# Kernel optimization log

Hardware: AMD Instinct MI355X
Metric: run time of the kernel (lower is better)

The kernel has to match this reference:

```python
import jax, jax.numpy as jnp
import numpy as np

B = 32768
INPUT_DIM = 2048
D = 2
HIDDEN = 128
V = 20          # output_dim (number of heads)
P = 6           # n_corr_params
R = 10          # r_lora = min(V // 2, 10)


def setup_inputs() -> dict:
    key = jax.random.key(0)
    ks = jax.random.split(key, 12)

    def lin(k, fan_in, shape):
        bound = 1.0 / np.sqrt(fan_in)
        return jax.random.uniform(k, shape, jnp.float32, -bound, bound)

    x = jax.random.normal(ks[0], (B, INPUT_DIM), jnp.float32)
    # encoder: Linear(input_dim, hidden) -> ReLU -> (Dropout=id) -> Linear(hidden, d)
    We1 = lin(ks[1], INPUT_DIM, (INPUT_DIM, HIDDEN))
    be1 = lin(ks[2], INPUT_DIM, (HIDDEN,))
    We2 = lin(ks[3], HIDDEN, (HIDDEN, D))
    be2 = lin(ks[4], HIDDEN, (D,))
    # 20 heads, each Linear(d, hidden) -> ReLU -> Linear(hidden, 6) -> Tanh,
    # stacked into batched weight tensors.
    W1 = lin(ks[5], D, (V, D, HIDDEN))
    b1 = lin(ks[6], D, (V, HIDDEN))
    W2 = lin(ks[7], HIDDEN, (V, HIDDEN, P))
    b2 = lin(ks[8], HIDDEN, (V, P))
    # LoRA params
    lora_A = jax.random.normal(ks[9], (D, R), jnp.float32) * 0.01
    lora_B = jax.random.normal(ks[10], (R, V * P), jnp.float32) * 0.01
    return {"x": x, "We1": We1, "be1": be1, "We2": We2, "be2": be2,
            "W1": W1, "b1": b1, "W2": W2, "b2": b2,
            "lora_A": lora_A, "lora_B": lora_B}


def reference(x, We1, be1, We2, be2, W1, b1, W2, b2, lora_A, lora_B):
    # encoder (nonlinear reduction; dropout is identity in eval)
    z = jax.nn.relu(x @ We1 + be1) @ We2 + be2            # [B, D]
    # all 20 heads as batched GEMMs
    h = jax.nn.relu(jnp.einsum('bd,vdh->bvh', z, W1) + b1)  # [B, V, HIDDEN]
    heads = jnp.tanh(jnp.einsum('bvh,vhp->bvp', h, W2) + b2)  # [B, V, P]
    # LoRA contribution, then outer tanh (note: double tanh, faithful to source)
    lora = (z @ lora_A @ lora_B).reshape(-1, V, P)         # [B, V, P]
    out = jnp.tanh(heads + 0.15 * lora)
    return (out, z)
```

## Files before the change

### kernel.cpp

```cpp
#include <hip/hip_runtime.h>
#include <hip/hip_bf16.h>
#include <cstdint>
#include <cstddef>

#define BDIM   32768
#define KDIM   2048
#define NDIM   128
#define VHEADS 20
#define PDIM   6
#define RLORA  10

#define BK      64
#define NCHUNK  (KDIM / BK)
#define OUT_ELEMS   (BDIM * VHEADS * PDIM)
#define WS_W_BYTES  (KDIM * NDIM * 2)

typedef __attribute__((ext_vector_type(8))) __bf16 bf16x8;
typedef __attribute__((ext_vector_type(4))) float f32x4;
typedef __attribute__((ext_vector_type(2))) float f32x2;
typedef __attribute__((ext_vector_type(4))) unsigned int u32x4;

union FragU { bf16x8 b; u32x4 u; };

__device__ __forceinline__ unsigned int cvt_pk_bf16(float lo, float hi) {
  unsigned int r;
  asm("v_cvt_pk_bf16_f32 %0, %1, %2" : "=v"(r) : "v"(lo), "v"(hi));
  return r;
}

__device__ __forceinline__ void gload_lds16(const void* g, void* l) {
  __builtin_amdgcn_global_load_lds(
      (const __attribute__((address_space(1))) void*)(g),
      (__attribute__((address_space(3))) void*)(l), 16, 0, 0);
}

__device__ __forceinline__ float fast_tanh(float x) {
  float ax = fabsf(x);
  float e  = __expf(-2.0f * ax);
  float t  = __fdividef(1.0f - e, 1.0f + e);
  return copysignf(t, x);
}

__global__ __launch_bounds__(256)
void k0_pack(const float* __restrict__ We1,
             const float* __restrict__ lA,
             const float* __restrict__ lB,
             unsigned short* __restrict__ wsw,
             float* __restrict__ wsM) {
  if (blockIdx.x == 128) {
    int t = threadIdx.x;
    if (t < 2 * VHEADS * PDIM) {
      int d  = t / (VHEADS * PDIM);
      int vp = t - d * (VHEADS * PDIM);
      float s = 0.f;
#pragma unroll
      for (int r = 0; r < RLORA; ++r)
        s = fmaf(lA[d * RLORA + r], lB[r * (VHEADS * PDIM) + vp], s);
      wsM[t] = s;
    }
    return;
  }
  int t    = blockIdx.x * 256 + threadIdx.x;
  int lane = t & 63;
  int blk  = t >> 6;
  int ks   = blk & 1;
  int nt   = (blk >> 1) & 7;
  int c    = blk >> 4;
  int n    = nt * 16 + (lane & 15);
  int kb   = c * 64 + ks * 32 + (lane >> 4) * 8;

  unsigned int u[4];
#pragma unroll
  for (int q = 0; q < 4; ++q) {
    float f0 = We1[(size_t)(kb + 2 * q + 0) * NDIM + n];
    float f1 = We1[(size_t)(kb + 2 * q + 1) * NDIM + n];
    __hip_bfloat16 h0 = __float2bfloat16(f0);
    __hip_bfloat16 h1 = __float2bfloat16(f1);
    u[q] = (unsigned int)*reinterpret_cast<unsigned short*>(&h0) |
           ((unsigned int)*reinterpret_cast<unsigned short*>(&h1) << 16);
  }
  *reinterpret_cast<u32x4*>(wsw + (size_t)t * 8) = u32x4{u[0], u[1], u[2], u[3]};
}

__global__ __launch_bounds__(256, 2)
void k1_fused(const float* __restrict__ x,
              const unsigned short* __restrict__ wp,
              const float* __restrict__ be1,
              const float* __restrict__ We2,
              const float* __restrict__ be2,
              const float* __restrict__ W1,
              const float* __restrict__ b1,
              const float* __restrict__ W2,
              const float* __restrict__ b2,
              const float* __restrict__ M,
              float* __restrict__ out,
              float* __restrict__ zout) {
  __shared__ char ldsA[2][16384] __attribute__((aligned(16)));
  __shared__ char ldsB[2][16384] __attribute__((aligned(16)));
  __shared__ float zsh[64][2];

  const int tid  = threadIdx.x;
  const int lane = tid & 63;
  const int wv   = tid >> 6;
  const int l15  = lane & 15;
  const int kgrp = lane >> 4;
  const int blk  = blockIdx.x;

  const int arow_off = wv * 16 + (lane >> 4);
  const char* bsrc = (const char*)wp + lane * 16;

  f32x4 acc[8];
#pragma unroll
  for (int i = 0; i < 8; ++i) acc[i] = f32x4{0.f, 0.f, 0.f, 0.f};

  auto STAGE = [&](int b, int c) {
#pragma unroll
    for (int q = 0; q < 4; ++q) {
      int row = arow_off + q * 4;
      const float* asrc = x + ((size_t)(blk * 64 + row) * KDIM + c * BK
                               + (((l15 ^ (row & 7)) << 2)));
      gload_lds16(asrc, &ldsA[b][(wv * 4 + q) * 1024]);
    }
#pragma unroll
    for (int q = 0; q < 4; ++q) {
      gload_lds16(bsrc + (size_t)c * 16384 + (wv * 4 + q) * 1024,
                  &ldsB[b][(wv * 4 + q) * 1024]);
    }
  };

  auto COMPUTE = [&](int b) {
    const int row = wv * 16 + l15;
    const char* abase = &ldsA[b][row * 256];
    const int rx = (row & 7) << 4;
    f32x4 A0 = *(const f32x4*)(abase + (((kgrp * 2 + 0) << 4) ^ rx));
    f32x4 A1 = *(const f32x4*)(abase + (((kgrp * 2 + 1) << 4) ^ rx));
    f32x4 A2 = *(const f32x4*)(abase + 128 + (((kgrp * 2 + 0) << 4) ^ rx));
    f32x4 A3 = *(const f32x4*)(abase + 128 + (((kgrp * 2 + 1) << 4) ^ rx));
    FragU a0, a1;
    a0.u = u32x4{cvt_pk_bf16(A0.x, A0.y), cvt_pk_bf16(A0.z, A0.w),
                 cvt_pk_bf16(A1.x, A1.y), cvt_pk_bf16(A1.z, A1.w)};
    a1.u = u32x4{cvt_pk_bf16(A2.x, A2.y), cvt_pk_bf16(A2.z, A2.w),
                 cvt_pk_bf16(A3.x, A3.y), cvt_pk_bf16(A3.z, A3.w)};
    const char* bbase = &ldsB[b][lane * 16];
#pragma unroll
    for (int nt = 0; nt < 8; ++nt) {
      FragU b0, b1;
      b0.u = *(const u32x4*)(bbase + (nt * 2 + 0) * 1024);
      b1.u = *(const u32x4*)(bbase + (nt * 2 + 1) * 1024);
      acc[nt] = __builtin_amdgcn_mfma_f32_16x16x32_bf16(a0.b, b0.b, acc[nt], 0, 0, 0);
      acc[nt] = __builtin_amdgcn_mfma_f32_16x16x32_bf16(a1.b, b1.b, acc[nt], 0, 0, 0);
    }
  };

  STAGE(0, 0);
  STAGE(1, 1);

#pragma unroll 1
  for (int c = 0; c < NCHUNK; ++c) {
    int b = c & 1;
    if (c + 1 < NCHUNK) {
      asm volatile("s_waitcnt vmcnt(8)" ::: "memory");
    } else {
      asm volatile("s_waitcnt vmcnt(0)" ::: "memory");
    }
    __builtin_amdgcn_sched_barrier(0);
    __builtin_amdgcn_s_barrier();
    COMPUTE(b);
    __builtin_amdgcn_s_barrier();
    __builtin_amdgcn_sched_barrier(0);
    if (c + 2 < NCHUNK) STAGE(b, c + 2);
  }

  float part[4][2];
#pragma unroll
  for (int j = 0; j < 4; ++j) { part[j][0] = 0.f; part[j][1] = 0.f; }
#pragma unroll
  for (int nt = 0; nt < 8; ++nt) {
    int col = nt * 16 + l15;
    float bb = be1[col];
    float w0 = We2[col * 2 + 0];
    float w1 = We2[col * 2 + 1];
#pragma unroll
    for (int j = 0; j < 4; ++j) {
      float h = acc[nt][j] + bb;
      h = h > 0.f ? h : 0.f;
      part[j][0] = fmaf(h, w0, part[j][0]);
      part[j][1] = fmaf(h, w1, part[j][1]);
    }
  }
#pragma unroll
  for (int m = 1; m < 16; m <<= 1) {
#pragma unroll
    for (int j = 0; j < 4; ++j) {
      part[j][0] += __shfl_xor(part[j][0], m, 64);
      part[j][1] += __shfl_xor(part[j][1], m, 64);
    }
  }
  if (l15 == 0) {
    float bz0 = be2[0], bz1 = be2[1];
#pragma unroll
    for (int j = 0; j < 4; ++j) {
      int rl = wv * 16 + kgrp * 4 + j;
      float zz0 = part[j][0] + bz0;
      float zz1 = part[j][1] + bz1;
      zsh[rl][0] = zz0;
      zsh[rl][1] = zz1;
      f32x2 zz = {zz0, zz1};
      *(f32x2*)(zout + (size_t)(blk * 64 + rl) * 2) = zz;
    }
  }
  __syncthreads();

  const int wvu = __builtin_amdgcn_readfirstlane(wv);
  float z0 = zsh[lane][0];
  float z1 = zsh[lane][1];
  float* orow = out + (size_t)(blk * 64 + lane) * (VHEADS * PDIM);

#pragma unroll 1
  for (int i = 0; i < 5; ++i) {
    int v = i * 4 + wvu;
    const float* w1a = W1 + (size_t)(v * 2 + 0) * NDIM;
    const float* w1b = W1 + (size_t)(v * 2 + 1) * NDIM;
    const float* bb1 = b1 + (size_t)v * NDIM;
    const float* w2  = W2 + (size_t)v * NDIM * PDIM;

    float p[6] = {0.f, 0.f, 0.f, 0.f, 0.f, 0.f};
#pragma unroll 4
    for (int h = 0; h < NDIM; ++h) {
      float hv = fmaf(z0, w1a[h], fmaf(z1, w1b[h], bb1[h]));
      hv = hv > 0.f ? hv : 0.f;
#pragma unroll
      for (int j = 0; j < 6; ++j) p[j] = fmaf(hv, w2[h * 6 + j], p[j]);
    }
    float o[6];
#pragma unroll
    for (int j = 0; j < 6; ++j) {
      float t1 = fast_tanh(p[j] + b2[v * PDIM + j]);
      float lo = fmaf(z0, M[v * PDIM + j], z1 * M[VHEADS * PDIM + v * PDIM + j]);
      o[j] = fast_tanh(fmaf(0.15f, lo, t1));
    }
    float* op = orow + v * PDIM;
    f32x2 o01 = {o[0], o[1]};
    f32x2 o23 = {o[2], o[3]};
    f32x2 o45 = {o[4], o[5]};
    __builtin_nontemporal_store(o01, (f32x2*)(op + 0));
    __builtin_nontemporal_store(o23, (f32x2*)(op + 2));
    __builtin_nontemporal_store(o45, (f32x2*)(op + 4));
  }
}

extern "C" void kernel_launch(void* const* d_in, const int* in_sizes, int n_in,
                              void* d_out, int out_size, void* d_ws, size_t ws_size,
                              hipStream_t stream) {
  const float* x   = (const float*)d_in[0];
  const float* We1 = (const float*)d_in[1];
  const float* be1 = (const float*)d_in[2];
  const float* We2 = (const float*)d_in[3];
  const float* be2 = (const float*)d_in[4];
  const float* W1  = (const float*)d_in[5];
  const float* b1  = (const float*)d_in[6];
  const float* W2  = (const float*)d_in[7];
  const float* b2  = (const float*)d_in[8];
  const float* lA  = (const float*)d_in[9];
  const float* lB  = (const float*)d_in[10];

  float* out  = (float*)d_out;
  float* zout = out + OUT_ELEMS;
  unsigned short* wsw = (unsigned short*)d_ws;
  float* wsM = (float*)((char*)d_ws + WS_W_BYTES);

  hipLaunchKernelGGL(k0_pack, dim3(129), dim3(256), 0, stream,
                     We1, lA, lB, wsw, wsM);
  hipLaunchKernelGGL(k1_fused, dim3(BDIM / 64), dim3(256), 0, stream,
                     x, wsw, be1, We2, be2, W1, b1, W2, b2, wsM, out, zout);
}
```

Baseline: 119.4 us.

## Shrink row tile to one 64-thread wave per 16 rows with barrier-free pipeline

```diff
diff --git a/kernel.cpp b/kernel.cpp
--- a/kernel.cpp
+++ b/kernel.cpp
@@ -10,8 +10,9 @@
 #define PDIM   6
 #define RLORA  10
 
-#define BK      64
-#define NCHUNK  (KDIM / BK)
+#define BM     16
+#define BK     64
+#define NCH    (KDIM / BK)
 #define OUT_ELEMS   (BDIM * VHEADS * PDIM)
 #define WS_W_BYTES  (KDIM * NDIM * 2)
 
@@ -82,7 +83,7 @@
   *reinterpret_cast<u32x4*>(wsw + (size_t)t * 8) = u32x4{u[0], u[1], u[2], u[3]};
 }
 
-__global__ __launch_bounds__(256, 2)
+__global__ __launch_bounds__(64)
 void k1_fused(const float* __restrict__ x,
               const unsigned short* __restrict__ wp,
               const float* __restrict__ be1,
@@ -95,80 +96,76 @@
               const float* __restrict__ M,
               float* __restrict__ out,
               float* __restrict__ zout) {
-  __shared__ char ldsA[2][16384] __attribute__((aligned(16)));
-  __shared__ char ldsB[2][16384] __attribute__((aligned(16)));
-  __shared__ float zsh[64][2];
-
-  const int tid  = threadIdx.x;
-  const int lane = tid & 63;
-  const int wv   = tid >> 6;
+  __shared__ char A0[4096] __attribute__((aligned(16)));
+  __shared__ char A1[4096] __attribute__((aligned(16)));
+  __shared__ char B0[16384] __attribute__((aligned(16)));
+  __shared__ char B1[16384] __attribute__((aligned(16)));
+
+  const int lane = threadIdx.x;
   const int l15  = lane & 15;
   const int kgrp = lane >> 4;
   const int blk  = blockIdx.x;
 
-  const int arow_off = wv * 16 + (lane >> 4);
-  const char* bsrc = (const char*)wp + lane * 16;
+  const float* xb = x + (size_t)blk * BM * KDIM;
 
   f32x4 acc[8];
 #pragma unroll
   for (int i = 0; i < 8; ++i) acc[i] = f32x4{0.f, 0.f, 0.f, 0.f};
 
-  auto STAGE = [&](int b, int c) {
+  auto STAGE = [&](char* Ad, char* Bd, int c) {
 #pragma unroll
     for (int q = 0; q < 4; ++q) {
-      int row = arow_off + q * 4;
-      const float* asrc = x + ((size_t)(blk * 64 + row) * KDIM + c * BK
-                               + (((l15 ^ (row & 7)) << 2)));
-      gload_lds16(asrc, &ldsA[b][(wv * 4 + q) * 1024]);
-    }
-#pragma unroll
-    for (int q = 0; q < 4; ++q) {
-      gload_lds16(bsrc + (size_t)c * 16384 + (wv * 4 + q) * 1024,
-                  &ldsB[b][(wv * 4 + q) * 1024]);
+      int row = q * 4 + (lane >> 4);
+      const float* s = xb + (size_t)row * KDIM + c * BK
+                       + (((lane & 15) ^ (row & 7)) << 2);
+      gload_lds16(s, Ad + q * 1024);
+    }
+#pragma unroll
+    for (int i = 0; i < 16; ++i) {
+      gload_lds16((const char*)wp + (size_t)c * 16384 + i * 1024 + lane * 16,
+                  Bd + i * 1024);
     }
   };
 
-  auto COMPUTE = [&](int b) {
-    const int row = wv * 16 + l15;
-    const char* abase = &ldsA[b][row * 256];
-    const int rx = (row & 7) << 4;
-    f32x4 A0 = *(const f32x4*)(abase + (((kgrp * 2 + 0) << 4) ^ rx));
-    f32x4 A1 = *(const f32x4*)(abase + (((kgrp * 2 + 1) << 4) ^ rx));
-    f32x4 A2 = *(const f32x4*)(abase + 128 + (((kgrp * 2 + 0) << 4) ^ rx));
-    f32x4 A3 = *(const f32x4*)(abase + 128 + (((kgrp * 2 + 1) << 4) ^ rx));
+  auto COMPUTE = [&](const char* Ad, const char* Bd) {
+    const char* ab = Ad + l15 * 256;
+    const int rx = l15 & 7;
+    f32x4 lo0 = *(const f32x4*)(ab + (((kgrp * 2 + 0) ^ rx) << 4));
+    f32x4 hi0 = *(const f32x4*)(ab + (((kgrp * 2 + 1) ^ rx) << 4));
+    f32x4 lo1 = *(const f32x4*)(ab + ((((kgrp * 2 + 0) ^ rx) + 8) << 4));
+    f32x4 hi1 = *(const f32x4*)(ab + ((((kgrp * 2 + 1) ^ rx) + 8) << 4));
     FragU a0, a1;
-    a0.u = u32x4{cvt_pk_bf16(A0.x, A0.y), cvt_pk_bf16(A0.z, A0.w),
-                 cvt_pk_bf16(A1.x, A1.y), cvt_pk_bf16(A1.z, A1.w)};
-    a1.u = u32x4{cvt_pk_bf16(A2.x, A2.y), cvt_pk_bf16(A2.z, A2.w),
-                 cvt_pk_bf16(A3.x, A3.y), cvt_pk_bf16(A3.z, A3.w)};
-    const char* bbase = &ldsB[b][lane * 16];
+    a0.u = u32x4{cvt_pk_bf16(lo0.x, lo0.y), cvt_pk_bf16(lo0.z, lo0.w),
+                 cvt_pk_bf16(hi0.x, hi0.y), cvt_pk_bf16(hi0.z, hi0.w)};
+    a1.u = u32x4{cvt_pk_bf16(lo1.x, lo1.y), cvt_pk_bf16(lo1.z, lo1.w),
+                 cvt_pk_bf16(hi1.x, hi1.y), cvt_pk_bf16(hi1.z, hi1.w)};
+    const char* bb = Bd + lane * 16;
 #pragma unroll
     for (int nt = 0; nt < 8; ++nt) {
       FragU b0, b1;
-      b0.u = *(const u32x4*)(bbase + (nt * 2 + 0) * 1024);
-      b1.u = *(const u32x4*)(bbase + (nt * 2 + 1) * 1024);
+      b0.u = *(const u32x4*)(bb + (nt * 2 + 0) * 1024);
+      b1.u = *(const u32x4*)(bb + (nt * 2 + 1) * 1024);
       acc[nt] = __builtin_amdgcn_mfma_f32_16x16x32_bf16(a0.b, b0.b, acc[nt], 0, 0, 0);
       acc[nt] = __builtin_amdgcn_mfma_f32_16x16x32_bf16(a1.b, b1.b, acc[nt], 0, 0, 0);
     }
   };
 
-  STAGE(0, 0);
-  STAGE(1, 1);
+  STAGE(A0, B0, 0);
 
 #pragma unroll 1
-  for (int c = 0; c < NCHUNK; ++c) {
-    int b = c & 1;
-    if (c + 1 < NCHUNK) {
-      asm volatile("s_waitcnt vmcnt(8)" ::: "memory");
+  for (int cc = 0; cc < NCH / 2; ++cc) {
+    STAGE(A1, B1, 2 * cc + 1);
+    asm volatile("s_waitcnt vmcnt(20)" ::: "memory");
+    __builtin_amdgcn_sched_barrier(0);
+    COMPUTE(A0, B0);
+    if (cc + 1 < NCH / 2) {
+      STAGE(A0, B0, 2 * cc + 2);
+      asm volatile("s_waitcnt vmcnt(20)" ::: "memory");
     } else {
       asm volatile("s_waitcnt vmcnt(0)" ::: "memory");
     }
     __builtin_amdgcn_sched_barrier(0);
-    __builtin_amdgcn_s_barrier();
-    COMPUTE(b);
-    __builtin_amdgcn_s_barrier();
-    __builtin_amdgcn_sched_barrier(0);
-    if (c + 2 < NCHUNK) STAGE(b, c + 2);
+    COMPUTE(A1, B1);
   }
 
   float part[4][2];
@@ -196,29 +193,31 @@
       part[j][1] += __shfl_xor(part[j][1], m, 64);
     }
   }
+  float* zf = (float*)A0;
   if (l15 == 0) {
     float bz0 = be2[0], bz1 = be2[1];
 #pragma unroll
     for (int j = 0; j < 4; ++j) {
-      int rl = wv * 16 + kgrp * 4 + j;
+      int rl = kgrp * 4 + j;
       float zz0 = part[j][0] + bz0;
       float zz1 = part[j][1] + bz1;
-      zsh[rl][0] = zz0;
-      zsh[rl][1] = zz1;
+      zf[rl * 2 + 0] = zz0;
+      zf[rl * 2 + 1] = zz1;
       f32x2 zz = {zz0, zz1};
-      *(f32x2*)(zout + (size_t)(blk * 64 + rl) * 2) = zz;
+      *(f32x2*)(zout + (size_t)(blk * BM + rl) * 2) = zz;
     }
   }
   __syncthreads();
 
-  const int wvu = __builtin_amdgcn_readfirstlane(wv);
-  float z0 = zsh[lane][0];
-  float z1 = zsh[lane][1];
-  float* orow = out + (size_t)(blk * 64 + lane) * (VHEADS * PDIM);
+  const int srow = l15;
+  const int slot = kgrp;
+  float z0 = zf[srow * 2 + 0];
+  float z1 = zf[srow * 2 + 1];
+  float* orow = out + (size_t)(blk * BM + srow) * (VHEADS * PDIM);
 
 #pragma unroll 1
   for (int i = 0; i < 5; ++i) {
-    int v = i * 4 + wvu;
+    int v = i * 4 + slot;
     const float* w1a = W1 + (size_t)(v * 2 + 0) * NDIM;
     const float* w1b = W1 + (size_t)(v * 2 + 1) * NDIM;
     const float* bb1 = b1 + (size_t)v * NDIM;
@@ -271,6 +270,6 @@
 
   hipLaunchKernelGGL(k0_pack, dim3(129), dim3(256), 0, stream,
                      We1, lA, lB, wsw, wsM);
-  hipLaunchKernelGGL(k1_fused, dim3(BDIM / 64), dim3(256), 0, stream,
+  hipLaunchKernelGGL(k1_fused, dim3(BDIM / BM), dim3(64), 0, stream,
                      x, wsw, be1, We2, be2, W1, b1, W2, b2, wsM, out, zout);
 }
```

After: 182.0 us. 52.3% more time.
